# Performance work log

Hardware: AMD Instinct MI355X
Metric: run time of the kernel (lower is better)

The kernel has to match this reference:

```python
import jax, jax.numpy as jnp
import numpy as np


def _layer_norm(x, w, b, eps=1e-5):
    mu = jnp.mean(x, axis=-1, keepdims=True)
    xc = x - mu
    var = jnp.mean(xc * xc, axis=-1, keepdims=True)
    return xc * jax.lax.rsqrt(var + eps) * w + b


def setup_inputs() -> dict:
    key = jax.random.key(0)
    ks = jax.random.split(key, 6)
    S, B, H = 2048, 2, 1024
    NH, NKV, HD = 16, 4, 64
    E, K, F = 8, 2, 4096
    w = lambda k, shape: 0.02 * jax.random.normal(k, shape, dtype=jnp.float32)
    return {
        "hidden_states": jax.random.normal(ks[0], (S, B, H), dtype=jnp.float32),
        "ln1_weight": jnp.ones((H,), jnp.float32),
        "ln1_bias": jnp.zeros((H,), jnp.float32),
        "ln2_weight": jnp.ones((H,), jnp.float32),
        "ln2_bias": jnp.zeros((H,), jnp.float32),
        "qkv_weight": w(ks[1], (H, (NH + 2 * NKV) * HD)),
        "proj_weight": w(ks[2], (H, H)),
        "router_weight": w(ks[3], (H, E)),
        "moe_w1": w(ks[4], (E, H, F)),
        "moe_w2": w(ks[5], (E, F, H)),
        "num_heads": NH,
        "num_kv_heads": NKV,
        "top_k": K,
    }


def reference(hidden_states, ln1_weight, ln1_bias, ln2_weight, ln2_bias,
              qkv_weight, proj_weight, router_weight, moe_w1, moe_w2,
              num_heads, num_kv_heads, top_k):
    S, B, H = hidden_states.shape
    HD = H // num_heads
    scale = 1.0 / (HD ** 0.5)

    # --- LN1 -> QKV projection (GQA split) ---
    ln1 = _layer_norm(hidden_states, ln1_weight, ln1_bias)
    qkv = ln1 @ qkv_weight                               # [S,B,(NH+2NKV)*HD]
    q_end = num_heads * HD
    k_end = q_end + num_kv_heads * HD
    q = qkv[..., :q_end].reshape(S, B, num_heads, HD)
    k = qkv[..., q_end:k_end].reshape(S, B, num_kv_heads, HD)
    v = qkv[..., k_end:].reshape(S, B, num_kv_heads, HD)
    rep = num_heads // num_kv_heads                      # repeat_interleave on head dim
    k = jnp.repeat(k, rep, axis=2)
    v = jnp.repeat(v, rep, axis=2)

    # --- causal SDPA, layout [B,NH,S,HD] ---
    q_bf = q.transpose(1, 2, 0, 3)
    k_bf = k.transpose(1, 2, 0, 3)
    v_bf = v.transpose(1, 2, 0, 3)
    scores = jnp.einsum('bhqd,bhkd->bhqk', q_bf, k_bf) * scale
    causal = jnp.tril(jnp.ones((S, S), dtype=bool))
    scores = jnp.where(causal, scores, jnp.finfo(scores.dtype).min)
    p = jax.nn.softmax(scores, axis=-1)
    attn = jnp.einsum('bhqk,bhkd->bhqd', p, v_bf)
    attn_out = attn.transpose(2, 0, 1, 3).reshape(S, B, H)  # back to [S,B,H]

    # --- output projection + residual ---
    h_attn = hidden_states + attn_out @ proj_weight

    # --- LN2 -> router top-k -> expert FFN -> weighted combine ---
    ln2 = _layer_norm(h_attn, ln2_weight, ln2_bias)
    T = S * B
    x = ln2.reshape(T, H)
    logits = x @ router_weight                           # [T,E]
    probs = jax.nn.softmax(logits, axis=-1)
    top_p, top_i = jax.lax.top_k(probs, top_k)           # [T,K]

    def expert_fn(_, w):
        w1, w2 = w
        return None, jax.nn.gelu(x @ w1, approximate=False) @ w2  # [T,H]

    _, outs = jax.lax.scan(expert_fn, None, (moe_w1, moe_w2))     # [E,T,H]
    gathered = outs[top_i, jnp.arange(T)[:, None], :]             # [T,K,H]
    moe_out = jnp.sum(gathered * top_p[..., None].astype(outs.dtype), axis=1)

    return h_attn + moe_out.reshape(S, B, H)
```

## Files before the change

### kernel.cpp

```cpp
#include <hip/hip_runtime.h>
#include <hip/hip_bf16.h>

constexpr int TT   = 4096;
constexpr int HH   = 1024;
constexpr int QKVN = 1536;
constexpr int FF   = 4096;

using f16x8  = __attribute__((ext_vector_type(8))) _Float16;
using f16x4  = __attribute__((ext_vector_type(4))) _Float16;
using bf16x8 = __attribute__((ext_vector_type(8))) short;
using s16x4  = __attribute__((ext_vector_type(4))) short;
using f32x4  = __attribute__((ext_vector_type(4))) float;

static __device__ __forceinline__ f32x4 mfma16(f16x8 a, f16x8 b, f32x4 c) {
  return __builtin_amdgcn_mfma_f32_16x16x32_f16(a, b, c, 0, 0, 0);
}
static __device__ __forceinline__ f32x4 mfmabf(bf16x8 a, bf16x8 b, f32x4 c) {
  return __builtin_amdgcn_mfma_f32_16x16x32_bf16(a, b, c, 0, 0, 0);
}
static __device__ __forceinline__ short f2bf(float f) {
  union { float f; unsigned u; } v; v.f = f;
  unsigned r = v.u + 0x7fffu + ((v.u >> 16) & 1u);
  return (short)(r >> 16);
}
static __device__ __forceinline__ void split16(float f, _Float16 &h, _Float16 &l) {
  _Float16 hh = (_Float16)f; h = hh; l = (_Float16)(f - (float)hh);
}
static __device__ __forceinline__ void gload16(const void* g, void* l) {
  __builtin_amdgcn_global_load_lds((__attribute__((address_space(1))) void*)(g),
                                   (__attribute__((address_space(3))) void*)(l), 16, 0, 0);
}

__global__ void zero_cnt(int* cnt) { if (threadIdx.x < 8) cnt[threadIdx.x] = 0; }

__global__ __launch_bounds__(256) void wconv_split(const float* __restrict__ W,
    _Float16* __restrict__ oh, _Float16* __restrict__ ol, int K, int N)
{
  __shared__ float ts[64][68];
  int n0 = blockIdx.x * 64, k0 = blockIdx.y * 64, t = threadIdx.x;
  #pragma unroll
  for (int it = 0; it < 4; it++) {
    int el = it * 1024 + t * 4; int r = el >> 6, c = el & 63;
    float4 v = *(const float4*)&W[(size_t)(k0 + r) * N + n0 + c];
    *(float4*)&ts[r][c] = v;
  }
  __syncthreads();
  #pragma unroll
  for (int it = 0; it < 4; it++) {
    int el = it * 1024 + t * 4; int nr = el >> 6, kc = el & 63;
    f16x4 hv, lv;
    #pragma unroll
    for (int q = 0; q < 4; q++) { _Float16 hh, ll; split16(ts[kc + q][nr], hh, ll); hv[q] = hh; lv[q] = ll; }
    size_t o = (size_t)(n0 + nr) * K + k0 + kc;
    *(f16x4*)&oh[o] = hv; *(f16x4*)&ol[o] = lv;
  }
}

__global__ __launch_bounds__(256) void wconv_bf(const float* __restrict__ W,
    short* __restrict__ o, int K, int N)
{
  __shared__ float ts[64][68];
  const float* Wz = W + (size_t)blockIdx.z * K * N;
  short* oz = o + (size_t)blockIdx.z * K * N;
  int n0 = blockIdx.x * 64, k0 = blockIdx.y * 64, t = threadIdx.x;
  #pragma unroll
  for (int it = 0; it < 4; it++) {
    int el = it * 1024 + t * 4; int r = el >> 6, c = el & 63;
    float4 v = *(const float4*)&Wz[(size_t)(k0 + r) * N + n0 + c];
    *(float4*)&ts[r][c] = v;
  }
  __syncthreads();
  #pragma unroll
  for (int it = 0; it < 4; it++) {
    int el = it * 1024 + t * 4; int nr = el >> 6, kc = el & 63;
    s16x4 bv;
    #pragma unroll
    for (int q = 0; q < 4; q++) bv[q] = f2bf(ts[kc + q][nr]);
    *(s16x4*)&oz[(size_t)(n0 + nr) * K + k0 + kc] = bv;
  }
}

__global__ __launch_bounds__(256) void vtrans(const float* __restrict__ qkv,
    _Float16* __restrict__ vh, _Float16* __restrict__ vl)
{
  __shared__ float ts[64][68];
  int bkv = blockIdx.x, b = bkv >> 2, kvh = bkv & 3;
  int s0 = blockIdx.y * 64, t = threadIdx.x;
  #pragma unroll
  for (int it = 0; it < 4; it++) {
    int el = it * 1024 + t * 4; int r = el >> 6, c = el & 63;
    float4 v = *(const float4*)&qkv[(size_t)((s0 + r) * 2 + b) * QKVN + 1280 + kvh * 64 + c];
    *(float4*)&ts[r][c] = v;
  }
  __syncthreads();
  #pragma unroll
  for (int it = 0; it < 4; it++) {
    int el = it * 1024 + t * 4; int d = el >> 6, sc = el & 63;
    f16x4 hv, lv;
    #pragma unroll
    for (int q = 0; q < 4; q++) { _Float16 hh, ll; split16(ts[sc + q][d], hh, ll); hv[q] = hh; lv[q] = ll; }
    size_t o = ((size_t)bkv * 64 + d) * 2048 + s0 + sc;
    *(f16x4*)&vh[o] = hv; *(f16x4*)&vl[o] = lv;
  }
}

template<int MODE>
__global__ __launch_bounds__(256) void ln_split(const float* __restrict__ in,
    const float* __restrict__ wt, const float* __restrict__ bs,
    _Float16* __restrict__ oh, _Float16* __restrict__ ol,
    float* __restrict__ xo, short* __restrict__ xbo)
{
  int row = blockIdx.x, tid = threadIdx.x;
  const float4* ip = (const float4*)(in + (size_t)row * HH);
  float4 v = ip[tid];
  float s = v.x + v.y + v.z + v.w;
  #pragma unroll
  for (int m = 1; m < 64; m <<= 1) s += __shfl_xor(s, m, 64);
  __shared__ float red1[4], red2[4];
  int wid = tid >> 6;
  if ((tid & 63) == 0) red1[wid] = s;
  __syncthreads();
  float mu = (red1[0] + red1[1] + red1[2] + red1[3]) * (1.0f / HH);
  float4 c; c.x = v.x - mu; c.y = v.y - mu; c.z = v.z - mu; c.w = v.w - mu;
  float s2 = c.x*c.x + c.y*c.y + c.z*c.z + c.w*c.w;
  #pragma unroll
  for (int m = 1; m < 64; m <<= 1) s2 += __shfl_xor(s2, m, 64);
  if ((tid & 63) == 0) red2[wid] = s2;
  __syncthreads();
  float ve = (red2[0] + red2[1] + red2[2] + red2[3]) * (1.0f / HH) + 1e-5f;
  float rs = rsqrtf(ve);
  rs = rs * (1.5f - 0.5f * ve * rs * rs);
  float4 wv = ((const float4*)wt)[tid], bv = ((const float4*)bs)[tid];
  float o4[4];
  o4[0] = c.x * rs * wv.x + bv.x; o4[1] = c.y * rs * wv.y + bv.y;
  o4[2] = c.z * rs * wv.z + bv.z; o4[3] = c.w * rs * wv.w + bv.w;
  size_t base = (size_t)row * HH + tid * 4;
  if (MODE == 0) {
    f16x4 hv, lv;
    #pragma unroll
    for (int q = 0; q < 4; q++) { _Float16 hh, ll; split16(o4[q], hh, ll); hv[q] = hh; lv[q] = ll; }
    *(f16x4*)&oh[base] = hv; *(f16x4*)&ol[base] = lv;
  } else {
    float4 ov; ov.x = o4[0]; ov.y = o4[1]; ov.z = o4[2]; ov.w = o4[3];
    *(float4*)&xo[base] = ov;
    s16x4 bvv;
    #pragma unroll
    for (int q = 0; q < 4; q++) bvv[q] = f2bf(o4[q]);
    *(s16x4*)&xbo[base] = bvv;
  }
}

template<int EPI>
__global__ __launch_bounds__(256) void gemm_split2(
    const _Float16* __restrict__ Agh, const _Float16* __restrict__ Agl,
    const _Float16* __restrict__ Bgh, const _Float16* __restrict__ Bgl,
    int K, float* __restrict__ C, int ldc, const float* __restrict__ resid,
    _Float16* __restrict__ kh, _Float16* __restrict__ kl)
{
  __shared__ _Float16 AhS[4096], AlS[4096], BhS[4096], BlS[4096];
  const int tid = threadIdx.x, lane = tid & 63, w = tid >> 6;
  const int wr = w >> 1, wc = w & 1;
  const int m0 = blockIdx.y * 128, n0 = blockIdx.x * 128;
  f32x4 acc[4][4] = {};
  const _Float16 *pah[2], *pal[2], *pbh[2], *pbl[2];
  int ldsb[2];
  #pragma unroll
  for (int i = 0; i < 2; i++) {
    int E = i * 2048 + w * 512 + lane * 8;
    int r = E >> 5, cc = E & 31;
    int cs = cc ^ ((r & 3) << 3);
    pah[i] = Agh + (size_t)(m0 + r) * K + cs;
    pal[i] = Agl + (size_t)(m0 + r) * K + cs;
    pbh[i] = Bgh + (size_t)(n0 + r) * K + cs;
    pbl[i] = Bgl + (size_t)(n0 + r) * K + cs;
    ldsb[i] = i * 2048 + w * 512;
  }
  const int rr = lane & 15, ko = (lane >> 4) * 8;
  const int xo = (rr & 3) << 3;
  for (int k0 = 0; k0 < K; k0 += 32) {
    __syncthreads();
    #pragma unroll
    for (int i = 0; i < 2; i++) {
      gload16(pah[i] + k0, &AhS[ldsb[i]]);
      gload16(pal[i] + k0, &AlS[ldsb[i]]);
      gload16(pbh[i] + k0, &BhS[ldsb[i]]);
      gload16(pbl[i] + k0, &BlS[ldsb[i]]);
    }
    __syncthreads();
    f16x8 fah[4], fal[4], fbh[4], fbl[4];
    #pragma unroll
    for (int m = 0; m < 4; m++) {
      int ro = (wr * 64 + m * 16 + rr) * 32 + (ko ^ xo);
      fah[m] = *(const f16x8*)&AhS[ro];
      fal[m] = *(const f16x8*)&AlS[ro];
    }
    #pragma unroll
    for (int n = 0; n < 4; n++) {
      int ro = (wc * 64 + n * 16 + rr) * 32 + (ko ^ xo);
      fbh[n] = *(const f16x8*)&BhS[ro];
      fbl[n] = *(const f16x8*)&BlS[ro];
    }
    #pragma unroll
    for (int m = 0; m < 4; m++)
      #pragma unroll
      for (int n = 0; n < 4; n++) {
        acc[m][n] = mfma16(fah[m], fbh[n], acc[m][n]);
        acc[m][n] = mfma16(fah[m], fbl[n], acc[m][n]);
        acc[m][n] = mfma16(fal[m], fbh[n], acc[m][n]);
      }
  }
  int r0 = m0 + wr * 64 + (lane >> 4) * 4;
  int c0 = n0 + wc * 64 + (lane & 15);
  #pragma unroll
  for (int m = 0; m < 4; m++)
    #pragma unroll
    for (int n = 0; n < 4; n++)
      #pragma unroll
      for (int j = 0; j < 4; j++) {
        int tr = r0 + m * 16 + j, tc = c0 + n * 16;
        size_t idx = (size_t)tr * ldc + tc;
        float v = acc[m][n][j];
        if (EPI == 1) v += resid[idx];
        C[idx] = v;
        if (EPI == 0 && tc >= 1024 && tc < 1280) {
          int s = tr >> 1, bb = tr & 1;
          int kvh = (tc - 1024) >> 6, d = (tc - 1024) & 63;
          _Float16 hh, ll; split16(v, hh, ll);
          size_t kidx = ((size_t)(bb * 4 + kvh) * 2048 + s) * 64 + d;
          kh[kidx] = hh; kl[kidx] = ll;
        }
      }
}

__global__ __launch_bounds__(256) void attn2(const float* __restrict__ qkv,
    const _Float16* __restrict__ khg, const _Float16* __restrict__ klg,
    const _Float16* __restrict__ vhg, const _Float16* __restrict__ vlg,
    _Float16* __restrict__ aoh, _Float16* __restrict__ aol)
{
  __shared__ _Float16 KhS[4096], KlS[4096], VhS[4096], VlS[4096];
  __shared__ _Float16 Ph[64][72], Pl[64][72];
  int qt = blockIdx.x, bh = blockIdx.y;
  int h = bh >> 1, b = bh & 1, kvh = h >> 2, bkv = b * 4 + kvh;
  int q0 = qt * 64;
  int tid = threadIdx.x, lane = tid & 63, w = tid >> 6;
  int rr = lane & 15, ko = (lane >> 4) * 8;
  const int xo8 = (rr & 7) << 3;
  int qrow = q0 + w * 16 + rr;
  const float* qp = qkv + (size_t)(qrow * 2 + b) * QKVN + h * 64;
  f16x8 qh[2], ql[2];
  #pragma unroll
  for (int kk = 0; kk < 2; kk++) {
    const float4* p = (const float4*)(qp + kk * 32 + ko);
    float4 v0 = p[0], v1 = p[1];
    float tq[8] = {v0.x, v0.y, v0.z, v0.w, v1.x, v1.y, v1.z, v1.w};
    f16x8 hv, lv;
    #pragma unroll
    for (int q = 0; q < 8; q++) { _Float16 hh, ll; split16(tq[q], hh, ll); hv[q] = hh; lv[q] = ll; }
    qh[kk] = hv; ql[kk] = lv;
  }
  const _Float16 *pk[2][2], *pv[2][2];
  int ldsb[2];
  #pragma unroll
  for (int i = 0; i < 2; i++) {
    int E = i * 2048 + w * 512 + lane * 8;
    int r = E >> 6, cc = E & 63;
    int cs = cc ^ ((r & 7) << 3);
    pk[i][0] = khg + ((size_t)bkv * 2048 + r) * 64 + cs;
    pk[i][1] = klg + ((size_t)bkv * 2048 + r) * 64 + cs;
    pv[i][0] = vhg + ((size_t)bkv * 64 + r) * 2048 + cs;
    pv[i][1] = vlg + ((size_t)bkv * 64 + r) * 2048 + cs;
    ldsb[i] = i * 2048 + w * 512;
  }
  f32x4 o[4] = {};
  float mo[4] = {-1e30f, -1e30f, -1e30f, -1e30f};
  float lo[4] = {0.f, 0.f, 0.f, 0.f};
  for (int ks = 0; ks <= q0; ks += 64) {
    __syncthreads();
    #pragma unroll
    for (int i = 0; i < 2; i++) {
      gload16(pk[i][0] + (size_t)ks * 64, &KhS[ldsb[i]]);
      gload16(pk[i][1] + (size_t)ks * 64, &KlS[ldsb[i]]);
      gload16(pv[i][0] + ks, &VhS[ldsb[i]]);
      gload16(pv[i][1] + ks, &VlS[ldsb[i]]);
    }
    __syncthreads();
    f32x4 s[4] = {};
    #pragma unroll
    for (int n = 0; n < 4; n++)
      #pragma unroll
      for (int kk = 0; kk < 2; kk++) {
        int ro = (n * 16 + rr) * 64 + ((kk * 32 + ko) ^ xo8);
        f16x8 kbh = *(const f16x8*)&KhS[ro];
        f16x8 kbl = *(const f16x8*)&KlS[ro];
        s[n] = mfma16(qh[kk], kbh, s[n]);
        s[n] = mfma16(qh[kk], kbl, s[n]);
        s[n] = mfma16(ql[kk], kbh, s[n]);
      }
    bool diag = (ks == q0);
    int myrow = q0 + w * 16 + (lane >> 4) * 4;
    #pragma unroll
    for (int n = 0; n < 4; n++)
      #pragma unroll
      for (int j = 0; j < 4; j++) {
        float v = s[n][j] * 0.125f;
        if (diag && (ks + n * 16 + rr) > (myrow + j)) v = -1e30f;
        s[n][j] = v;
      }
    float mt[4];
    #pragma unroll
    for (int j = 0; j < 4; j++) mt[j] = fmaxf(fmaxf(s[0][j], s[1][j]), fmaxf(s[2][j], s[3][j]));
    #pragma unroll
    for (int msk = 1; msk < 16; msk <<= 1)
      #pragma unroll
      for (int j = 0; j < 4; j++) mt[j] = fmaxf(mt[j], __shfl_xor(mt[j], msk, 64));
    float pvv[4][4], rsum[4];
    #pragma unroll
    for (int j = 0; j < 4; j++) {
      float mn = fmaxf(mo[j], mt[j]);
      float al = expf(mo[j] - mn);
      mo[j] = mn;
      rsum[j] = 0.f;
      #pragma unroll
      for (int n = 0; n < 4; n++) { float pp = expf(s[n][j] - mn); pvv[n][j] = pp; rsum[j] += pp; }
      lo[j] *= al;
      #pragma unroll
      for (int n = 0; n < 4; n++) o[n][j] *= al;
    }
    #pragma unroll
    for (int msk = 1; msk < 16; msk <<= 1)
      #pragma unroll
      for (int j = 0; j < 4; j++) rsum[j] += __shfl_xor(rsum[j], msk, 64);
    #pragma unroll
    for (int j = 0; j < 4; j++) lo[j] += rsum[j];
    int prow = w * 16 + (lane >> 4) * 4;
    #pragma unroll
    for (int n = 0; n < 4; n++)
      #pragma unroll
      for (int j = 0; j < 4; j++) {
        _Float16 hh, ll; split16(pvv[n][j], hh, ll);
        Ph[prow + j][n * 16 + rr] = hh;
        Pl[prow + j][n * 16 + rr] = ll;
      }
    #pragma unroll
    for (int kk = 0; kk < 2; kk++) {
      f16x8 pah = *(const f16x8*)&Ph[w * 16 + rr][kk * 32 + ko];
      f16x8 pal = *(const f16x8*)&Pl[w * 16 + rr][kk * 32 + ko];
      #pragma unroll
      for (int dn = 0; dn < 4; dn++) {
        int ro = (dn * 16 + rr) * 64 + ((kk * 32 + ko) ^ xo8);
        f16x8 vbh = *(const f16x8*)&VhS[ro];
        f16x8 vbl = *(const f16x8*)&VlS[ro];
        o[dn] = mfma16(pah, vbh, o[dn]);
        o[dn] = mfma16(pah, vbl, o[dn]);
        o[dn] = mfma16(pal, vbh, o[dn]);
      }
    }
  }
  float inv[4];
  #pragma unroll
  for (int j = 0; j < 4; j++) inv[j] = 1.0f / lo[j];
  int orow = q0 + w * 16 + (lane >> 4) * 4;
  int ocol = h * 64 + rr;
  #pragma unroll
  for (int dn = 0; dn < 4; dn++)
    #pragma unroll
    for (int j = 0; j < 4; j++) {
      float v = o[dn][j] * inv[j];
      _Float16 hh, ll; split16(v, hh, ll);
      size_t idx = (size_t)((orow + j) * 2 + b) * HH + ocol + dn * 16;
      aoh[idx] = hh; aol[idx] = ll;
    }
}

__global__ __launch_bounds__(256) void router_kernel(const float* __restrict__ x,
    const float* __restrict__ rw, int* __restrict__ list, float* __restrict__ listp,
    int* __restrict__ cnt)
{
  __shared__ float rws[HH * 8];
  int tid = threadIdx.x;
  for (int i = tid; i < HH * 8; i += 256) rws[i] = rw[i];
  __syncthreads();
  int t = blockIdx.x * 4 + (tid >> 6);
  int lane = tid & 63;
  const float* xp = x + (size_t)t * HH;
  float acc[8] = {};
  for (int i = lane; i < HH; i += 64) {
    float xv = xp[i];
    #pragma unroll
    for (int e = 0; e < 8; e++) acc[e] += xv * rws[i * 8 + e];
  }
  #pragma unroll
  for (int e = 0; e < 8; e++)
    #pragma unroll
    for (int m = 1; m < 64; m <<= 1) acc[e] += __shfl_xor(acc[e], m, 64);
  if (lane == 0) {
    float mx = acc[0];
    #pragma unroll
    for (int e = 1; e < 8; e++) mx = fmaxf(mx, acc[e]);
    float p[8], sum = 0.f;
    #pragma unroll
    for (int e = 0; e < 8; e++) { p[e] = expf(acc[e] - mx); sum += p[e]; }
    float inv = 1.0f / sum;
    int i1 = 0; float v1 = acc[0];
    #pragma unroll
    for (int e = 1; e < 8; e++) if (acc[e] > v1) { v1 = acc[e]; i1 = e; }
    int i2 = -1; float v2 = -3.4e38f;
    #pragma unroll
    for (int e = 0; e < 8; e++) if (e != i1 && acc[e] > v2) { v2 = acc[e]; i2 = e; }
    int pos1 = atomicAdd(&cnt[i1], 1);
    list[i1 * TT + pos1] = t; listp[i1 * TT + pos1] = p[i1] * inv;
    int pos2 = atomicAdd(&cnt[i2], 1);
    list[i2 * TT + pos2] = t; listp[i2 * TT + pos2] = p[i2] * inv;
  }
}

__global__ __launch_bounds__(256) void moe1_full(const short* __restrict__ xbf,
    const short* __restrict__ w1T, const int* __restrict__ list,
    const int* __restrict__ cnt, short* __restrict__ hidden)
{
  int e = blockIdx.z;
  int ce = cnt[e];
  int off = 0;
  #pragma unroll
  for (int i = 0; i < 8; i++) if (i < e) off += cnt[i];
  int m0 = blockIdx.y * 128;
  if (m0 >= ce) return;
  int n0 = blockIdx.x * 128;
  __shared__ short AS[4096], BS[4096];
  const int tid = threadIdx.x, lane = tid & 63, w = tid >> 6;
  const int wr = w >> 1, wc = w & 1;
  f32x4 acc[4][4] = {};
  const short *pa[2], *pb[2];
  int ldsb[2];
  #pragma unroll
  for (int i = 0; i < 2; i++) {
    int E = i * 2048 + w * 512 + lane * 8;
    int r = E >> 5, cc = E & 31;
    int cs = cc ^ ((r & 3) << 3);
    int apos = m0 + r; if (apos > ce - 1) apos = ce - 1;
    int tok = list[e * TT + apos];
    pa[i] = xbf + (size_t)tok * HH + cs;
    pb[i] = w1T + ((size_t)e * FF + n0 + r) * HH + cs;
    ldsb[i] = i * 2048 + w * 512;
  }
  const int rr = lane & 15, ko = (lane >> 4) * 8;
  const int xo = (rr & 3) << 3;
  for (int k0 = 0; k0 < HH; k0 += 32) {
    __syncthreads();
    #pragma unroll
    for (int i = 0; i < 2; i++) {
      gload16(pa[i] + k0, &AS[ldsb[i]]);
      gload16(pb[i] + k0, &BS[ldsb[i]]);
    }
    __syncthreads();
    bf16x8 fa[4], fb[4];
    #pragma unroll
    for (int m = 0; m < 4; m++) fa[m] = *(const bf16x8*)&AS[(wr * 64 + m * 16 + rr) * 32 + (ko ^ xo)];
    #pragma unroll
    for (int n = 0; n < 4; n++) fb[n] = *(const bf16x8*)&BS[(wc * 64 + n * 16 + rr) * 32 + (ko ^ xo)];
    #pragma unroll
    for (int m = 0; m < 4; m++)
      #pragma unroll
      for (int n = 0; n < 4; n++) acc[m][n] = mfmabf(fa[m], fb[n], acc[m][n]);
  }
  int p0 = m0 + wr * 64 + (lane >> 4) * 4;
  int c0 = n0 + wc * 64 + (lane & 15);
  #pragma unroll
  for (int m = 0; m < 4; m++)
    #pragma unroll
    for (int n = 0; n < 4; n++)
      #pragma unroll
      for (int j = 0; j < 4; j++) {
        int pos = p0 + m * 16 + j;
        if (pos < ce) {
          float v = acc[m][n][j];
          v = 0.5f * v * (1.0f + erff(v * 0.70710678f));
          hidden[(size_t)(off + pos) * FF + c0 + n * 16] = f2bf(v);
        }
      }
}

__global__ __launch_bounds__(256) void moe2_full(const short* __restrict__ hidden,
    const short* __restrict__ w2T, const int* __restrict__ list,
    const float* __restrict__ listp, const int* __restrict__ cnt,
    float* __restrict__ outp)
{
  int e = blockIdx.z;
  int ce = cnt[e];
  int off = 0;
  #pragma unroll
  for (int i = 0; i < 8; i++) if (i < e) off += cnt[i];
  int m0 = blockIdx.y * 128;
  if (m0 >= ce) return;
  int n0 = blockIdx.x * 128;
  __shared__ short AS[4096], BS[4096];
  const int tid = threadIdx.x, lane = tid & 63, w = tid >> 6;
  const int wr = w >> 1, wc = w & 1;
  f32x4 acc[4][4] = {};
  const short *pa[2], *pb[2];
  int ldsb[2];
  #pragma unroll
  for (int i = 0; i < 2; i++) {
    int E = i * 2048 + w * 512 + lane * 8;
    int r = E >> 5, cc = E & 31;
    int cs = cc ^ ((r & 3) << 3);
    int apos = m0 + r; if (apos > ce - 1) apos = ce - 1;
    pa[i] = hidden + ((size_t)off + apos) * FF + cs;
    pb[i] = w2T + ((size_t)e * HH + n0 + r) * FF + cs;
    ldsb[i] = i * 2048 + w * 512;
  }
  const int rr = lane & 15, ko = (lane >> 4) * 8;
  const int xo = (rr & 3) << 3;
  for (int k0 = 0; k0 < FF; k0 += 32) {
    __syncthreads();
    #pragma unroll
    for (int i = 0; i < 2; i++) {
      gload16(pa[i] + k0, &AS[ldsb[i]]);
      gload16(pb[i] + k0, &BS[ldsb[i]]);
    }
    __syncthreads();
    bf16x8 fa[4], fb[4];
    #pragma unroll
    for (int m = 0; m < 4; m++) fa[m] = *(const bf16x8*)&AS[(wr * 64 + m * 16 + rr) * 32 + (ko ^ xo)];
    #pragma unroll
    for (int n = 0; n < 4; n++) fb[n] = *(const bf16x8*)&BS[(wc * 64 + n * 16 + rr) * 32 + (ko ^ xo)];
    #pragma unroll
    for (int m = 0; m < 4; m++)
      #pragma unroll
      for (int n = 0; n < 4; n++) acc[m][n] = mfmabf(fa[m], fb[n], acc[m][n]);
  }
  int p0 = m0 + wr * 64 + (lane >> 4) * 4;
  int c0 = n0 + wc * 64 + (lane & 15);
  #pragma unroll
  for (int m = 0; m < 4; m++)
    #pragma unroll
    for (int j = 0; j < 4; j++) {
      int pos = p0 + m * 16 + j;
      if (pos < ce) {
        int tk = list[e * TT + pos];
        float pw = listp[e * TT + pos];
        #pragma unroll
        for (int n = 0; n < 4; n++)
          atomicAdd(&outp[(size_t)tk * HH + c0 + n * 16], pw * acc[m][n][j]);
      }
    }
}

__global__ __launch_bounds__(256) void moe_gemm1(const float* __restrict__ x,
    const float* __restrict__ w1, const int* __restrict__ list,
    const int* __restrict__ cnt, short* __restrict__ hidden, int e)
{
  int ce = cnt[e];
  int m0 = blockIdx.y * 128;
  if (m0 >= ce) return;
  int n0 = blockIdx.x * 128;
  __shared__ short As[128][40], Bs[128][40];
  int tid = threadIdx.x, lane = tid & 63, w = tid >> 6, wr = w >> 1, wc = w & 1;
  f32x4 acc[4][4] = {};
  int arow = tid >> 1, akh = (tid & 1) * 16;
  int apos = m0 + arow;
  int tok = list[(size_t)e * TT + (apos < ce ? apos : 0)];
  const float* ap = x + (size_t)tok * HH + akh;
  int bn = tid & 127, bkh = (tid >> 7) * 16;
  const float* bp = w1 + (size_t)e * HH * FF + (size_t)bkh * FF + n0 + bn;
  for (int k0 = 0; k0 < HH; k0 += 32) {
    __syncthreads();
    {
      const float4* p = (const float4*)(ap + k0);
      bf16x8 s0, s1;
      #pragma unroll
      for (int q = 0; q < 2; q++) { float4 v = p[q]; s0[q*4] = f2bf(v.x); s0[q*4+1] = f2bf(v.y); s0[q*4+2] = f2bf(v.z); s0[q*4+3] = f2bf(v.w); }
      #pragma unroll
      for (int q = 0; q < 2; q++) { float4 v = p[q+2]; s1[q*4] = f2bf(v.x); s1[q*4+1] = f2bf(v.y); s1[q*4+2] = f2bf(v.z); s1[q*4+3] = f2bf(v.w); }
      *(bf16x8*)&As[arow][akh] = s0; *(bf16x8*)&As[arow][akh+8] = s1;
    }
    {
      const float* p = bp + (size_t)k0 * FF;
      bf16x8 s0, s1;
      #pragma unroll
      for (int q = 0; q < 8; q++) s0[q] = f2bf(p[(size_t)q * FF]);
      #pragma unroll
      for (int q = 0; q < 8; q++) s1[q] = f2bf(p[(size_t)(q+8) * FF]);
      *(bf16x8*)&Bs[bn][bkh] = s0; *(bf16x8*)&Bs[bn][bkh+8] = s1;
    }
    __syncthreads();
    int rr = lane & 15, ko = (lane >> 4) * 8;
    bf16x8 fa[4], fb[4];
    #pragma unroll
    for (int m = 0; m < 4; m++) fa[m] = *(bf16x8*)&As[wr*64 + m*16 + rr][ko];
    #pragma unroll
    for (int n = 0; n < 4; n++) fb[n] = *(bf16x8*)&Bs[wc*64 + n*16 + rr][ko];
    #pragma unroll
    for (int m = 0; m < 4; m++)
      #pragma unroll
      for (int n = 0; n < 4; n++) acc[m][n] = mfmabf(fa[m], fb[n], acc[m][n]);
  }
  int p0 = m0 + wr*64 + (lane >> 4) * 4;
  int c0 = n0 + wc*64 + (lane & 15);
  #pragma unroll
  for (int m = 0; m < 4; m++)
    #pragma unroll
    for (int n = 0; n < 4; n++)
      #pragma unroll
      for (int j = 0; j < 4; j++) {
        int pos = p0 + m*16 + j;
        if (pos < ce) {
          float v = acc[m][n][j];
          v = 0.5f * v * (1.0f + erff(v * 0.70710678f));
          hidden[(size_t)pos * FF + c0 + n*16] = f2bf(v);
        }
      }
}

__global__ __launch_bounds__(256) void moe_gemm2(const short* __restrict__ hidden,
    const float* __restrict__ w2, const int* __restrict__ list,
    const float* __restrict__ listp, const int* __restrict__ cnt,
    float* __restrict__ outp, int e)
{
  int ce = cnt[e];
  int m0 = blockIdx.y * 128;
  if (m0 >= ce) return;
  int n0 = blockIdx.x * 128;
  __shared__ short As[128][40], Bs[128][40];
  int tid = threadIdx.x, lane = tid & 63, w = tid >> 6, wr = w >> 1, wc = w & 1;
  f32x4 acc[4][4] = {};
  int arow = tid >> 1, akh = (tid & 1) * 16;
  int apos = m0 + arow;
  const short* ap = hidden + (size_t)(apos < ce ? apos : 0) * FF + akh;
  int bn = tid & 127, bkh = (tid >> 7) * 16;
  const float* bp = w2 + (size_t)e * FF * HH + (size_t)bkh * HH + n0 + bn;
  for (int k0 = 0; k0 < FF; k0 += 32) {
    __syncthreads();
    {
      const int4* p = (const int4*)(ap + k0);
      int4 a0 = p[0], a1 = p[1];
      *(int4*)&As[arow][akh]   = a0;
      *(int4*)&As[arow][akh+8] = a1;
    }
    {
      const float* p = bp + (size_t)k0 * HH;
      bf16x8 s0, s1;
      #pragma unroll
      for (int q = 0; q < 8; q++) s0[q] = f2bf(p[(size_t)q * HH]);
      #pragma unroll
      for (int q = 0; q < 8; q++) s1[q] = f2bf(p[(size_t)(q+8) * HH]);
      *(bf16x8*)&Bs[bn][bkh] = s0; *(bf16x8*)&Bs[bn][bkh+8] = s1;
    }
    __syncthreads();
    int rr = lane & 15, ko = (lane >> 4) * 8;
    bf16x8 fa[4], fb[4];
    #pragma unroll
    for (int m = 0; m < 4; m++) fa[m] = *(bf16x8*)&As[wr*64 + m*16 + rr][ko];
    #pragma unroll
    for (int n = 0; n < 4; n++) fb[n] = *(bf16x8*)&Bs[wc*64 + n*16 + rr][ko];
    #pragma unroll
    for (int m = 0; m < 4; m++)
      #pragma unroll
      for (int n = 0; n < 4; n++) acc[m][n] = mfmabf(fa[m], fb[n], acc[m][n]);
  }
  int p0 = m0 + wr*64 + (lane >> 4) * 4;
  int c0 = n0 + wc*64 + (lane & 15);
  #pragma unroll
  for (int m = 0; m < 4; m++)
    #pragma unroll
    for (int j = 0; j < 4; j++) {
      int pos = p0 + m*16 + j;
      if (pos < ce) {
        int tk = list[(size_t)e * TT + pos];
        float pw = listp[(size_t)e * TT + pos];
        #pragma unroll
        for (int n = 0; n < 4; n++)
          atomicAdd(&outp[(size_t)tk * HH + c0 + n*16], pw * acc[m][n][j]);
      }
    }
}

extern "C" void kernel_launch(void* const* d_in, const int* in_sizes, int n_in,
                              void* d_out, int out_size, void* d_ws, size_t ws_size,
                              hipStream_t stream)
{
  const float* hs      = (const float*)d_in[0];
  const float* ln1w    = (const float*)d_in[1];
  const float* ln1b    = (const float*)d_in[2];
  const float* ln2w    = (const float*)d_in[3];
  const float* ln2b    = (const float*)d_in[4];
  const float* qkvw    = (const float*)d_in[5];
  const float* projw   = (const float*)d_in[6];
  const float* routerw = (const float*)d_in[7];
  const float* w1      = (const float*)d_in[8];
  const float* w2      = (const float*)d_in[9];
  float* out = (float*)d_out;

  const size_t MB = 1024 * 1024;
  char* wsb = (char*)d_ws;
  bool full = ws_size >= 153 * MB;

  float*    qkvbuf = (float*)wsb;
  _Float16* khb    = (_Float16*)(wsb + 24 * MB);
  _Float16* klb    = (_Float16*)(wsb + 26 * MB);
  _Float16* vhb    = (_Float16*)(wsb + 28 * MB);
  _Float16* vlb    = (_Float16*)(wsb + 30 * MB);
  short*    hidden = (short*)wsb;
  size_t r2 = full ? 64 * MB : 32 * MB;
  _Float16* ln1h = (_Float16*)(wsb + r2);
  _Float16* ln1l = (_Float16*)(wsb + r2 + 8 * MB);
  _Float16* aohb = ln1h;
  _Float16* aolb = ln1l;
  float*    xbuf = (float*)(wsb + r2);
  short*    xbf  = (short*)(wsb + r2 + 16 * MB);
  size_t r3 = full ? 88 * MB : 56 * MB;
  _Float16* qkvwTh  = (_Float16*)(wsb + r3);
  _Float16* qkvwTl  = (_Float16*)(wsb + r3 + 3 * MB);
  _Float16* projwTh = (_Float16*)(wsb + r3 + 6 * MB);
  _Float16* projwTl = (_Float16*)(wsb + r3 + 8 * MB);
  short*    w1T     = (short*)(wsb + r3);
  short*    w2T     = (short*)(wsb + r3);
  size_t r4 = full ? 152 * MB : 66 * MB;
  int*   list  = (int*)(wsb + r4);
  float* listp = (float*)(wsb + r4 + 128 * 1024);
  int*   cnt   = (int*)(wsb + r4 + 256 * 1024);

  zero_cnt<<<1, 64, 0, stream>>>(cnt);
  wconv_split<<<dim3(QKVN / 64, HH / 64), 256, 0, stream>>>(qkvw, qkvwTh, qkvwTl, HH, QKVN);
  wconv_split<<<dim3(HH / 64, HH / 64), 256, 0, stream>>>(projw, projwTh, projwTl, HH, HH);
  ln_split<0><<<TT, 256, 0, stream>>>(hs, ln1w, ln1b, ln1h, ln1l, nullptr, nullptr);
  gemm_split2<0><<<dim3(QKVN / 128, TT / 128), 256, 0, stream>>>(
      ln1h, ln1l, qkvwTh, qkvwTl, HH, qkvbuf, QKVN, nullptr, khb, klb);
  vtrans<<<dim3(8, 32), 256, 0, stream>>>(qkvbuf, vhb, vlb);
  attn2<<<dim3(32, 32), 256, 0, stream>>>(qkvbuf, khb, klb, vhb, vlb, aohb, aolb);
  gemm_split2<1><<<dim3(HH / 128, TT / 128), 256, 0, stream>>>(
      aohb, aolb, projwTh, projwTl, HH, out, HH, hs, nullptr, nullptr);
  ln_split<1><<<TT, 256, 0, stream>>>(out, ln2w, ln2b, nullptr, nullptr, xbuf, xbf);
  router_kernel<<<TT / 4, 256, 0, stream>>>(xbuf, routerw, list, listp, cnt);
  if (full) {
    wconv_bf<<<dim3(FF / 64, HH / 64, 8), 256, 0, stream>>>(w1, w1T, HH, FF);
    moe1_full<<<dim3(FF / 128, TT / 128, 8), 256, 0, stream>>>(xbf, w1T, list, cnt, hidden);
    wconv_bf<<<dim3(HH / 64, FF / 64, 8), 256, 0, stream>>>(w2, w2T, FF, HH);
    moe2_full<<<dim3(HH / 128, TT / 128, 8), 256, 0, stream>>>(hidden, w2T, list, listp, cnt, out);
  } else {
    for (int e = 0; e < 8; e++) {
      moe_gemm1<<<dim3(FF / 128, TT / 128), 256, 0, stream>>>(xbuf, w1, list, cnt, hidden, e);
      moe_gemm2<<<dim3(HH / 128, TT / 128), 256, 0, stream>>>(hidden, w2, list, listp, cnt, out, e);
    }
  }
}
```

Before: 786.4 us.

## Double-buffer MoE GEMM LDS tiles, reorder attention blocks, raise MFMA priority

```diff
diff --git a/kernel.cpp b/kernel.cpp
--- a/kernel.cpp
+++ b/kernel.cpp
@@ -239,7 +239,8 @@
 {
   __shared__ _Float16 KhS[4096], KlS[4096], VhS[4096], VlS[4096];
   __shared__ _Float16 Ph[64][72], Pl[64][72];
-  int qt = blockIdx.x, bh = blockIdx.y;
+  int bh = blockIdx.x;
+  int qt = gridDim.y - 1 - blockIdx.y;
   int h = bh >> 1, b = bh & 1, kvh = h >> 2, bkv = b * 4 + kvh;
   int q0 = qt * 64;
   int tid = threadIdx.x, lane = tid & 63, w = tid >> 6;
@@ -285,6 +286,7 @@
     }
     __syncthreads();
     f32x4 s[4] = {};
+    __builtin_amdgcn_s_setprio(1);
     #pragma unroll
     for (int n = 0; n < 4; n++)
       #pragma unroll
@@ -296,6 +298,7 @@
         s[n] = mfma16(qh[kk], kbl, s[n]);
         s[n] = mfma16(ql[kk], kbh, s[n]);
       }
+    __builtin_amdgcn_s_setprio(0);
     bool diag = (ks == q0);
     int myrow = q0 + w * 16 + (lane >> 4) * 4;
     #pragma unroll
@@ -341,6 +344,7 @@
         Ph[prow + j][n * 16 + rr] = hh;
         Pl[prow + j][n * 16 + rr] = ll;
       }
+    __builtin_amdgcn_s_setprio(1);
     #pragma unroll
     for (int kk = 0; kk < 2; kk++) {
       f16x8 pah = *(const f16x8*)&Ph[w * 16 + rr][kk * 32 + ko];
@@ -355,6 +359,7 @@
         o[dn] = mfma16(pal, vbh, o[dn]);
       }
     }
+    __builtin_amdgcn_s_setprio(0);
   }
   float inv[4];
   #pragma unroll
@@ -426,7 +431,7 @@
   int m0 = blockIdx.y * 128;
   if (m0 >= ce) return;
   int n0 = blockIdx.x * 128;
-  __shared__ short AS[4096], BS[4096];
+  __shared__ short AS[2][4096], BS[2][4096];
   const int tid = threadIdx.x, lane = tid & 63, w = tid >> 6;
   const int wr = w >> 1, wc = w & 1;
   f32x4 acc[4][4] = {};
@@ -445,23 +450,35 @@
   }
   const int rr = lane & 15, ko = (lane >> 4) * 8;
   const int xo = (rr & 3) << 3;
+  #pragma unroll
+  for (int i = 0; i < 2; i++) {
+    gload16(pa[i], &AS[0][ldsb[i]]);
+    gload16(pb[i], &BS[0][ldsb[i]]);
+  }
+  __syncthreads();
+  int cb = 0;
   for (int k0 = 0; k0 < HH; k0 += 32) {
-    __syncthreads();
-    #pragma unroll
-    for (int i = 0; i < 2; i++) {
-      gload16(pa[i] + k0, &AS[ldsb[i]]);
-      gload16(pb[i] + k0, &BS[ldsb[i]]);
-    }
-    __syncthreads();
+    int nk = k0 + 32;
+    if (nk < HH) {
+      #pragma unroll
+      for (int i = 0; i < 2; i++) {
+        gload16(pa[i] + nk, &AS[cb ^ 1][ldsb[i]]);
+        gload16(pb[i] + nk, &BS[cb ^ 1][ldsb[i]]);
+      }
+    }
     bf16x8 fa[4], fb[4];
     #pragma unroll
-    for (int m = 0; m < 4; m++) fa[m] = *(const bf16x8*)&AS[(wr * 64 + m * 16 + rr) * 32 + (ko ^ xo)];
-    #pragma unroll
-    for (int n = 0; n < 4; n++) fb[n] = *(const bf16x8*)&BS[(wc * 64 + n * 16 + rr) * 32 + (ko ^ xo)];
+    for (int m = 0; m < 4; m++) fa[m] = *(const bf16x8*)&AS[cb][(wr * 64 + m * 16 + rr) * 32 + (ko ^ xo)];
+    #pragma unroll
+    for (int n = 0; n < 4; n++) fb[n] = *(const bf16x8*)&BS[cb][(wc * 64 + n * 16 + rr) * 32 + (ko ^ xo)];
+    __builtin_amdgcn_s_setprio(1);
     #pragma unroll
     for (int m = 0; m < 4; m++)
       #pragma unroll
       for (int n = 0; n < 4; n++) acc[m][n] = mfmabf(fa[m], fb[n], acc[m][n]);
+    __builtin_amdgcn_s_setprio(0);
+    __syncthreads();
+    cb ^= 1;
   }
   int p0 = m0 + wr * 64 + (lane >> 4) * 4;
   int c0 = n0 + wc * 64 + (lane & 15);
@@ -493,7 +510,7 @@
   int m0 = blockIdx.y * 128;
   if (m0 >= ce) return;
   int n0 = blockIdx.x * 128;
-  __shared__ short AS[4096], BS[4096];
+  __shared__ short AS[2][4096], BS[2][4096];
   const int tid = threadIdx.x, lane = tid & 63, w = tid >> 6;
   const int wr = w >> 1, wc = w & 1;
   f32x4 acc[4][4] = {};
@@ -511,23 +528,35 @@
   }
   const int rr = lane & 15, ko = (lane >> 4) * 8;
   const int xo = (rr & 3) << 3;
+  #pragma unroll
+  for (int i = 0; i < 2; i++) {
+    gload16(pa[i], &AS[0][ldsb[i]]);
+    gload16(pb[i], &BS[0][ldsb[i]]);
+  }
+  __syncthreads();
+  int cb = 0;
   for (int k0 = 0; k0 < FF; k0 += 32) {
-    __syncthreads();
-    #pragma unroll
-    for (int i = 0; i < 2; i++) {
-      gload16(pa[i] + k0, &AS[ldsb[i]]);
-      gload16(pb[i] + k0, &BS[ldsb[i]]);
-    }
-    __syncthreads();
+    int nk = k0 + 32;
+    if (nk < FF) {
+      #pragma unroll
+      for (int i = 0; i < 2; i++) {
+        gload16(pa[i] + nk, &AS[cb ^ 1][ldsb[i]]);
+        gload16(pb[i] + nk, &BS[cb ^ 1][ldsb[i]]);
+      }
+    }
     bf16x8 fa[4], fb[4];
     #pragma unroll
-    for (int m = 0; m < 4; m++) fa[m] = *(const bf16x8*)&AS[(wr * 64 + m * 16 + rr) * 32 + (ko ^ xo)];
-    #pragma unroll
-    for (int n = 0; n < 4; n++) fb[n] = *(const bf16x8*)&BS[(wc * 64 + n * 16 + rr) * 32 + (ko ^ xo)];
+    for (int m = 0; m < 4; m++) fa[m] = *(const bf16x8*)&AS[cb][(wr * 64 + m * 16 + rr) * 32 + (ko ^ xo)];
+    #pragma unroll
+    for (int n = 0; n < 4; n++) fb[n] = *(const bf16x8*)&BS[cb][(wc * 64 + n * 16 + rr) * 32 + (ko ^ xo)];
+    __builtin_amdgcn_s_setprio(1);
     #pragma unroll
     for (int m = 0; m < 4; m++)
       #pragma unroll
       for (int n = 0; n < 4; n++) acc[m][n] = mfmabf(fa[m], fb[n], acc[m][n]);
+    __builtin_amdgcn_s_setprio(0);
+    __syncthreads();
+    cb ^= 1;
   }
   int p0 = m0 + wr * 64 + (lane >> 4) * 4;
   int c0 = n0 + wc * 64 + (lane & 15);
```

Result: faster. 709.3 us (-9.8%).
